# Performance work log

Measured on AMD Instinct MI355X. Metric: run time of the kernel, lower is better.

## Reference

```python
import jax, jax.numpy as jnp
import numpy as np

B, T, D, H = 4, 2048, 768, 12
HD = D // H  # head size 64
DF = 3072    # feed-forward size


def setup_inputs() -> dict:
    key = jax.random.key(0)
    ks = jax.random.split(key, 10)
    s = 0.02
    return {
        "x": jax.random.normal(ks[0], (B, T, D), jnp.float32),
        "mask": jnp.ones((B, T), jnp.int32),
        "Wq": jax.random.normal(ks[1], (D, D), jnp.float32) * s,
        "bq": jnp.zeros((D,), jnp.float32),
        "Wk": jax.random.normal(ks[2], (D, D), jnp.float32) * s,
        "bk": jnp.zeros((D,), jnp.float32),
        "Wv": jax.random.normal(ks[3], (D, D), jnp.float32) * s,
        "bv": jnp.zeros((D,), jnp.float32),
        "Wo": jax.random.normal(ks[4], (D, D), jnp.float32) * s,
        "bo": jnp.zeros((D,), jnp.float32),
        "W1": jax.random.normal(ks[5], (D, DF), jnp.float32) * s,
        "b1": jnp.zeros((DF,), jnp.float32),
        "W2": jax.random.normal(ks[6], (DF, D), jnp.float32) * s,
        "b2": jnp.zeros((D,), jnp.float32),
    }


def reference(x, mask, Wq, bq, Wk, bk, Wv, bv, Wo, bo, W1, b1, W2, b2):
    scale = 1.0 / np.sqrt(HD).astype(np.float32)
    # projections -> [B, H, T, HD]
    def split_heads(t):
        return t.reshape(B, T, H, HD).transpose(0, 2, 1, 3)
    q = split_heads(x @ Wq + bq)
    k = split_heads(x @ Wk + bk)
    v = split_heads(x @ Wv + bv)
    # [B, H, T, T] attention scores (materialized, as in the original)
    scores = jnp.einsum('bhqd,bhkd->bhqk', q, k) * scale
    neg_inf = jnp.float32(-jnp.inf)
    scores = jnp.where(mask[:, None, None, :] == 0, neg_inf, scores)
    attn = jax.nn.softmax(scores, axis=-1)
    ctx = jnp.einsum('bhqk,bhkd->bhqd', attn, v)          # [B,H,T,HD]
    ctx = ctx.transpose(0, 2, 1, 3).reshape(B, T, D)       # merge heads
    attn_out = ctx @ Wo + bo
    h = x + attn_out                                       # residual 1 (dropout p=0)
    ff = jax.nn.gelu(h @ W1 + b1, approximate=False) @ W2 + b2
    out = h + ff                                           # residual 2
    return out, attn
```

## Files before the change

### kernel.cpp

```cpp
#include <hip/hip_runtime.h>
#include <hip/hip_bf16.h>
#include <math.h>

typedef unsigned short u16;
typedef __attribute__((ext_vector_type(8))) short short8;
typedef __attribute__((ext_vector_type(4))) float f32x4;

constexpr int Bc = 4, Tt = 2048, Dd = 768, Hh = 12, Hd = 64, Df = 3072;
constexpr int BT = Bc * Tt;

__device__ __forceinline__ u16 f2b(float x) {
  __hip_bfloat16 h = __float2bfloat16(x);
  return *reinterpret_cast<u16*>(&h);
}
__device__ __forceinline__ float b2f(u16 v) {
  unsigned int u = ((unsigned int)v) << 16;
  return __builtin_bit_cast(float, u);
}
__device__ __forceinline__ float gelu_exact(float g) {
  return 0.5f * g * (1.0f + erff(g * 0.70710678118654752440f));
}
__device__ __forceinline__ void gload16(const void* g, void* l) {
  __builtin_amdgcn_global_load_lds(
      (const __attribute__((address_space(1))) unsigned int*)g,
      (__attribute__((address_space(3))) unsigned int*)l, 16, 0, 0);
}

__device__ __forceinline__ void tr_tile(const float* __restrict__ in,
                                        u16* __restrict__ out, int R, int C,
                                        int bx, int by, float* sh) {
  const int tx = threadIdx.x & 31, ty = threadIdx.x >> 5;
  const int r0 = by * 32, c0 = bx * 32;
#pragma unroll
  for (int i = 0; i < 4; ++i)
    sh[(ty + i * 8) * 33 + tx] = in[(size_t)(r0 + ty + i * 8) * C + c0 + tx];
  __syncthreads();
#pragma unroll
  for (int i = 0; i < 4; ++i)
    out[(size_t)(c0 + ty + i * 8) * R + r0 + tx] = f2b(sh[tx * 33 + ty + i * 8]);
}

__global__ __launch_bounds__(256) void prep_all(
    const float* __restrict__ x, const float* __restrict__ Wq,
    const float* __restrict__ Wk, const float* __restrict__ Wv,
    const float* __restrict__ Wo, const float* __restrict__ W1,
    const float* __restrict__ W2, const float* __restrict__ bq,
    const float* __restrict__ bk, const float* __restrict__ bv,
    const int* __restrict__ mask, u16* __restrict__ xb,
    u16* __restrict__ wqkvT, u16* __restrict__ woT, u16* __restrict__ w1T,
    u16* __restrict__ w2T, float* __restrict__ biasc,
    unsigned int* __restrict__ mwords) {
  __shared__ float sh[32 * 33];
  const int s = blockIdx.x;
  if (s < 3072) {
    int i = (s * 256 + threadIdx.x) * 8;
    float4 a = *(const float4*)&x[i];
    float4 b = *(const float4*)&x[i + 4];
    u16 t[8] = {f2b(a.x), f2b(a.y), f2b(a.z), f2b(a.w),
                f2b(b.x), f2b(b.y), f2b(b.z), f2b(b.w)};
    *(uint4*)&xb[i] = *(uint4*)t;
  } else if (s < 3648) {
    int u = s - 3072; tr_tile(Wq, wqkvT, Dd, Dd, u % 24, u / 24, sh);
  } else if (s < 4224) {
    int u = s - 3648; tr_tile(Wk, wqkvT + 768 * Dd, Dd, Dd, u % 24, u / 24, sh);
  } else if (s < 4800) {
    int u = s - 4224; tr_tile(Wv, wqkvT + 1536 * Dd, Dd, Dd, u % 24, u / 24, sh);
  } else if (s < 5376) {
    int u = s - 4800; tr_tile(Wo, woT, Dd, Dd, u % 24, u / 24, sh);
  } else if (s < 7680) {
    int u = s - 5376; tr_tile(W1, w1T, Dd, Df, u % 96, u / 96, sh);
  } else if (s < 9984) {
    int u = s - 7680; tr_tile(W2, w2T, Df, Dd, u % 24, u / 24, sh);
  } else if (s < 9993) {
    int i = (s - 9984) * 256 + threadIdx.x;
    biasc[i] = (i < 768) ? bq[i] : (i < 1536) ? bk[i - 768] : bv[i - 1536];
  } else {
    const int id = threadIdx.x;
    const int b_ = id >> 6, kv0 = (id & 63) * 32;
    unsigned int wbits = 0u;
    for (int j = 0; j < 32; ++j)
      wbits |= (mask[b_ * Tt + kv0 + j] ? 1u : 0u) << j;
    mwords[id] = wbits;
  }
}

template <int MODE>
__global__ __launch_bounds__(256) void mgemm(
    const u16* __restrict__ A, const u16* __restrict__ Bt,
    const float* __restrict__ bias, const float* __restrict__ add,
    const u16* __restrict__ addb, void* __restrict__ C0,
    void* __restrict__ C1, void* __restrict__ C2, int K, int N) {
  __shared__ __align__(16) u16 As[3][128 * 32];
  __shared__ __align__(16) u16 Bs[3][128 * 32];
  const int tid = threadIdx.x;
  const int lane = tid & 63, wv = tid >> 6;
  const int m0 = blockIdx.y * 128, n0 = blockIdx.x * 128;
  const int wm = (wv >> 1) * 64, wn = (wv & 1) * 64;

  f32x4 acc[4][4] = {};

#define MG_STAGE(k0_, bf_)                                                    \
  {                                                                           \
    _Pragma("unroll") for (int i_ = 0; i_ < 2; ++i_) {                        \
      const int idx_ = i_ * 256 + tid;                                        \
      const int row_ = idx_ >> 2;                                             \
      const int kc_ = (idx_ & 3) * 8;                                         \
      const u16* ga_;                                                         \
      if constexpr (MODE == 2) {                                              \
        const int m_ = m0 + row_, b_ = m_ >> 11, t_ = m_ & 2047;              \
        const int kk_ = (k0_) + kc_, hd_ = kk_ >> 6, d_ = kk_ & 63;           \
        ga_ = &A[(((size_t)(b_ * Hh + hd_) * Tt + t_) << 6) + d_];            \
      } else {                                                                \
        ga_ = &A[(size_t)(m0 + row_) * K + (k0_) + kc_];                      \
      }                                                                       \
      gload16(ga_, &As[bf_][idx_ * 8]);                                       \
      gload16(&Bt[(size_t)(n0 + row_) * K + (k0_) + kc_], &Bs[bf_][idx_ * 8]);\
    }                                                                         \
  }
#define FENCE() asm volatile("" ::: "memory")

  const int nsteps = K >> 5;
  MG_STAGE(0, 0);
  MG_STAGE(32, 1);

  for (int it = 0; it < nsteps; ++it) {
    if (it + 1 < nsteps)
      asm volatile("s_waitcnt vmcnt(4)" ::: "memory");
    else
      asm volatile("s_waitcnt vmcnt(0)" ::: "memory");
    __builtin_amdgcn_s_barrier();
    FENCE();
    const int cur = it % 3;
    if (it + 2 < nsteps) {
      const int nb = (it + 2) % 3;
      MG_STAGE((it + 2) * 32, nb);
    }
    short8 af[4], bfr[4];
#pragma unroll
    for (int i = 0; i < 4; ++i) {
      af[i] = *reinterpret_cast<const short8*>(
          &As[cur][(wm + i * 16 + (lane & 15)) * 32 + (lane >> 4) * 8]);
      bfr[i] = *reinterpret_cast<const short8*>(
          &Bs[cur][(wn + i * 16 + (lane & 15)) * 32 + (lane >> 4) * 8]);
    }
    __builtin_amdgcn_s_setprio(1);
#pragma unroll
    for (int i = 0; i < 4; ++i)
#pragma unroll
      for (int j = 0; j < 4; ++j)
        acc[i][j] = __builtin_amdgcn_mfma_f32_16x16x32_bf16(af[i], bfr[j],
                                                            acc[i][j], 0, 0, 0);
    __builtin_amdgcn_s_setprio(0);
  }
#undef MG_STAGE
#undef FENCE

  const int lr = (lane >> 4) * 4, lc = lane & 15;
#pragma unroll
  for (int i = 0; i < 4; ++i) {
    const int mbase = m0 + wm + i * 16 + lr;
#pragma unroll
    for (int j = 0; j < 4; ++j) {
      const int col = n0 + wn + j * 16 + lc;
      const float bvs = bias[col];
#pragma unroll
      for (int r = 0; r < 4; ++r) {
        const int m = mbase + r;
        float g = acc[i][j][r] + bvs;
        if constexpr (MODE == 5) {
          const int b = m >> 11, t = m & 2047;
          if (col < 768) {
            const int head = col >> 6, d = col & 63;
            ((u16*)C0)[(((size_t)(b * Hh + head) * Tt + t) << 6) + d] = f2b(g);
          } else if (col < 1536) {
            const int c = col - 768, head = c >> 6, d = c & 63;
            ((u16*)C1)[(((size_t)(b * Hh + head) * Tt + t) << 6) + d] = f2b(g);
          } else {
            const int c = col - 1536, head = c >> 6, d = c & 63;
            ((u16*)C2)[(((size_t)(b * Hh + head) * Hd + d) << 11) + t] = f2b(g);
          }
        } else if constexpr (MODE == 2) {
          g += add[(size_t)m * Dd + col];
          ((u16*)C0)[(size_t)m * Dd + col] = f2b(g);
        } else if constexpr (MODE == 3) {
          ((u16*)C0)[(size_t)m * N + col] = f2b(gelu_exact(g));
        } else {
          g += b2f(addb[(size_t)m * Dd + col]);
          ((float*)C0)[(size_t)m * Dd + col] = g;
        }
      }
    }
  }
}

__global__ __launch_bounds__(256) void attn_fused(
    const u16* __restrict__ qb, const u16* __restrict__ kb,
    const u16* __restrict__ vtb, const unsigned int* __restrict__ mwords,
    float* __restrict__ attn, u16* __restrict__ ctxb) {
  const int bh = blockIdx.y;
  const int b = bh / Hh;
  const int q0 = blockIdx.x * 64;
  const u16* Qg = qb + (size_t)bh * Tt * Hd;
  const u16* Kg = kb + (size_t)bh * Tt * Hd;
  const u16* Vg = vtb + (size_t)bh * Hd * Tt;
  float* attng = attn + (size_t)bh * Tt * Tt;
  u16* ctxg = ctxb + (size_t)bh * Tt * Hd;
  const unsigned int* mwp = mwords + b * 64;

  __shared__ __align__(16) u16 Ks[2][128 * 64];
  __shared__ __align__(16) u16 Vs[64 * 128];
  __shared__ __align__(16) float Pf[64 * 128];

  const int tid = threadIdx.x, lane = tid & 63, wv = tid >> 6;
  const int lc = lane & 15, lg = lane >> 4;
  const int ql = wv * 16 + lc;
  const int qsw = lc & 7;

#define STAGE_K(t, bf)                                                       \
  {                                                                          \
    const int kv0_ = (t) * 128;                                              \
    _Pragma("unroll") for (int w_ = 0; w_ < 4; ++w_) {                       \
      const int p_ = w_ * 256 + tid;                                         \
      const int row_ = p_ >> 3, kc8_ = (p_ & 7) ^ (row_ & 7);                \
      gload16(Kg + (size_t)(kv0_ + row_) * Hd + kc8_ * 8, &Ks[bf][p_ * 8]);  \
    }                                                                        \
  }
#define STAGE_V(t)                                                           \
  {                                                                          \
    const int kv0_ = (t) * 128;                                              \
    _Pragma("unroll") for (int w_ = 0; w_ < 4; ++w_) {                       \
      const int p_ = w_ * 256 + tid;                                         \
      const int d_ = p_ >> 4, pc_ = (p_ & 15) ^ (d_ & 7);                    \
      gload16(Vg + (size_t)d_ * Tt + kv0_ + pc_ * 8, &Vs[p_ * 8]);           \
    }                                                                        \
  }
#define FENCE() asm volatile("" ::: "memory")

  short8 qf[2];
#pragma unroll
  for (int ks = 0; ks < 2; ++ks)
    qf[ks] = *(const short8*)&Qg[(size_t)(q0 + ql) * Hd + ks * 32 + lg * 8];

  float l = 0.f;

  STAGE_K(0, 0);
  for (int t = 0; t < 16; ++t) {
    asm volatile("s_waitcnt vmcnt(0)" ::: "memory");
    __builtin_amdgcn_s_barrier();
    FENCE();
    const int bf = t & 1;
    if (t < 15) STAGE_K(t + 1, bf ^ 1);
    f32x4 s[8] = {};
#pragma unroll
    for (int ks = 0; ks < 2; ++ks) {
      const int ph = (ks * 4 + lg) ^ qsw;
#pragma unroll
      for (int i = 0; i < 8; ++i) {
        const short8 af = *(const short8*)&Ks[bf][(i * 16 + lc) * 64 + ph * 8];
        s[i] = __builtin_amdgcn_mfma_f32_16x16x32_bf16(af, qf[ks], s[i], 0, 0, 0);
      }
    }
    const uint4 mw4 = *(const uint4*)&mwp[t * 4];
    const unsigned int mwa[4] = {mw4.x, mw4.y, mw4.z, mw4.w};
    float ts = 0.f;
#pragma unroll
    for (int i = 0; i < 8; ++i) {
      const unsigned int w = mwa[i >> 1];
#pragma unroll
      for (int r = 0; r < 4; ++r) {
        const float bit = (float)((w >> ((i & 1) * 16 + lg * 4 + r)) & 1u);
        ts += __expf(s[i][r] * 0.125f) * bit;
      }
    }
    ts += __shfl_xor(ts, 16);
    ts += __shfl_xor(ts, 32);
    l += ts;
  }

  const float linv = 1.f / l;
  f32x4 cacc[4] = {};

  __builtin_amdgcn_s_barrier();
  FENCE();

  STAGE_K(0, 0);
  STAGE_V(0);
  for (int t = 0; t < 16; ++t) {
    const int kv0 = t * 128;
    const int bf = t & 1;
    if (t == 0)
      asm volatile("s_waitcnt vmcnt(0)" ::: "memory");
    else
      asm volatile("s_waitcnt vmcnt(8)" ::: "memory");
    __builtin_amdgcn_s_barrier();
    FENCE();
    if (t < 15) STAGE_K(t + 1, bf ^ 1);
    f32x4 s[8] = {};
#pragma unroll
    for (int ks = 0; ks < 2; ++ks) {
      const int ph = (ks * 4 + lg) ^ qsw;
#pragma unroll
      for (int i = 0; i < 8; ++i) {
        const short8 af = *(const short8*)&Ks[bf][(i * 16 + lc) * 64 + ph * 8];
        s[i] = __builtin_amdgcn_mfma_f32_16x16x32_bf16(af, qf[ks], s[i], 0, 0, 0);
      }
    }
    const uint4 mw4 = *(const uint4*)&mwp[t * 4];
    const unsigned int mwa[4] = {mw4.x, mw4.y, mw4.z, mw4.w};
#pragma unroll
    for (int i = 0; i < 8; ++i) {
      const unsigned int w = mwa[i >> 1];
      float pv[4];
#pragma unroll
      for (int r = 0; r < 4; ++r) {
        const float bit = (float)((w >> ((i & 1) * 16 + lg * 4 + r)) & 1u);
        pv[r] = __expf(s[i][r] * 0.125f) * bit * linv;
      }
      const int g = (i * 4 + lg) ^ qsw;
      *(f32x4*)&Pf[ql * 128 + g * 4] = *(f32x4*)pv;
    }
#pragma unroll
    for (int ks = 0; ks < 4; ++ks) {
      const int gA = (ks * 8 + lg * 2) ^ qsw;
      const int gB = (ks * 8 + lg * 2 + 1) ^ qsw;
      const f32x4 fA = *(const f32x4*)&Pf[ql * 128 + gA * 4];
      const f32x4 fB = *(const f32x4*)&Pf[ql * 128 + gB * 4];
      u16 pb[8] = {f2b(fA[0]), f2b(fA[1]), f2b(fA[2]), f2b(fA[3]),
                   f2b(fB[0]), f2b(fB[1]), f2b(fB[2]), f2b(fB[3])};
      const short8 pa = *(const short8*)pb;
#pragma unroll
      for (int j2 = 0; j2 < 4; ++j2) {
        const int d = j2 * 16 + lc;
        const short8 vb2 =
            *(const short8*)&Vs[d * 128 + (((ks * 4 + lg) ^ (d & 7))) * 8];
        cacc[j2] =
            __builtin_amdgcn_mfma_f32_16x16x32_bf16(pa, vb2, cacc[j2], 0, 0, 0);
      }
    }
    __builtin_amdgcn_s_barrier();
    FENCE();
    if (t < 15) STAGE_V(t + 1);
#pragma unroll
    for (int it = 0; it < 8; ++it) {
      const int row = wv * 16 + it * 2 + (lane >> 5);
      const int colg = lane & 31;
      const int g2 = colg ^ (row & 7);
      const f32x4 v = *(const f32x4*)&Pf[row * 128 + g2 * 4];
      __builtin_nontemporal_store(
          v, (f32x4*)&attng[(size_t)(q0 + row) * Tt + kv0 + colg * 4]);
    }
  }

#pragma unroll
  for (int j2 = 0; j2 < 4; ++j2)
#pragma unroll
    for (int r = 0; r < 4; ++r) {
      const int q = q0 + wv * 16 + lg * 4 + r;
      ctxg[(size_t)q * Hd + j2 * 16 + lc] = f2b(cacc[j2][r]);
    }
#undef STAGE_K
#undef STAGE_V
#undef FENCE
}

extern "C" void kernel_launch(void* const* d_in, const int* in_sizes, int n_in,
                              void* d_out, int out_size, void* d_ws,
                              size_t ws_size, hipStream_t stream) {
  const float* x = (const float*)d_in[0];
  const int* mask = (const int*)d_in[1];
  const float* Wq = (const float*)d_in[2];
  const float* bq = (const float*)d_in[3];
  const float* Wk = (const float*)d_in[4];
  const float* bk = (const float*)d_in[5];
  const float* Wv = (const float*)d_in[6];
  const float* bv = (const float*)d_in[7];
  const float* Wo = (const float*)d_in[8];
  const float* bo = (const float*)d_in[9];
  const float* W1 = (const float*)d_in[10];
  const float* b1 = (const float*)d_in[11];
  const float* W2 = (const float*)d_in[12];
  const float* b2 = (const float*)d_in[13];

  float* out = (float*)d_out;
  float* attn = out + (size_t)BT * Dd;

  char* w = (char*)d_ws;
  u16* xb = (u16*)w;      w += (size_t)BT * Dd * 2;
  u16* wqkvT = (u16*)w;   w += (size_t)Dd * 2304 * 2;
  u16* woT = (u16*)w;     w += (size_t)Dd * Dd * 2;
  u16* w1T = (u16*)w;     w += (size_t)Dd * Df * 2;
  u16* w2T = (u16*)w;     w += (size_t)Df * Dd * 2;
  float* biasc = (float*)w;            w += 2304 * 4;
  unsigned int* mwords = (unsigned int*)w; w += 256 * 4;
  u16* qb = (u16*)w;      w += (size_t)BT * Dd * 2;
  u16* kb = (u16*)w;      w += (size_t)BT * Dd * 2;
  u16* vtb = (u16*)w;     w += (size_t)BT * Dd * 2;
  u16* ctxb = (u16*)w;    w += (size_t)BT * Dd * 2;
  u16* ff1b = (u16*)w;    w += (size_t)BT * Df * 2;
  u16* hb = vtb;

  dim3 blk(256);

  prep_all<<<dim3(9994), blk, 0, stream>>>(x, Wq, Wk, Wv, Wo, W1, W2, bq, bk,
                                           bv, mask, xb, wqkvT, woT, w1T, w2T,
                                           biasc, mwords);

  mgemm<5><<<dim3(18, 64), blk, 0, stream>>>(xb, wqkvT, biasc, nullptr, nullptr,
                                             qb, kb, vtb, Dd, 2304);

  attn_fused<<<dim3(32, 48), blk, 0, stream>>>(qb, kb, vtb, mwords, attn, ctxb);

  mgemm<2><<<dim3(6, 64), blk, 0, stream>>>(ctxb, woT, bo, x, nullptr, hb,
                                            nullptr, nullptr, Dd, Dd);

  mgemm<3><<<dim3(24, 64), blk, 0, stream>>>(hb, w1T, b1, nullptr, nullptr,
                                             ff1b, nullptr, nullptr, Dd, Df);

  mgemm<4><<<dim3(6, 64), blk, 0, stream>>>(ff1b, w2T, b2, nullptr, hb, out,
                                            nullptr, nullptr, Df, Dd);
}
```

Baseline: 480.9 us.

## Double-buffer V and store P as bf16 in attention; simplify GEMM pipeline

The attention kernel now keeps the probability tile in shared memory as bf16 rather than fp32, halving that buffer and removing a separate conversion pass before the PV MFMA. V is double-buffered and prefetched together with K, which removes one block barrier per KV tile. The GEMM changes from a three-stage global_load_lds pipeline with explicit vmcnt waits and s_setprio to a plain two-stage double buffer with __syncthreads. The fp32 attention-probability output is now rebuilt from bf16-rounded values, which lowers its precision, and the simpler GEMM pipeline may hide memory latency less well.

```diff
diff --git a/kernel.cpp b/kernel.cpp
--- a/kernel.cpp
+++ b/kernel.cpp
@@ -90,8 +90,8 @@
     const float* __restrict__ bias, const float* __restrict__ add,
     const u16* __restrict__ addb, void* __restrict__ C0,
     void* __restrict__ C1, void* __restrict__ C2, int K, int N) {
-  __shared__ __align__(16) u16 As[3][128 * 32];
-  __shared__ __align__(16) u16 Bs[3][128 * 32];
+  __shared__ __align__(16) u16 As[2][128 * 32];
+  __shared__ __align__(16) u16 Bs[2][128 * 32];
   const int tid = threadIdx.x;
   const int lane = tid & 63, wv = tid >> 6;
   const int m0 = blockIdx.y * 128, n0 = blockIdx.x * 128;
@@ -117,24 +117,14 @@
       gload16(&Bt[(size_t)(n0 + row_) * K + (k0_) + kc_], &Bs[bf_][idx_ * 8]);\
     }                                                                         \
   }
-#define FENCE() asm volatile("" ::: "memory")
-
-  const int nsteps = K >> 5;
+
   MG_STAGE(0, 0);
-  MG_STAGE(32, 1);
-
-  for (int it = 0; it < nsteps; ++it) {
-    if (it + 1 < nsteps)
-      asm volatile("s_waitcnt vmcnt(4)" ::: "memory");
-    else
-      asm volatile("s_waitcnt vmcnt(0)" ::: "memory");
-    __builtin_amdgcn_s_barrier();
-    FENCE();
-    const int cur = it % 3;
-    if (it + 2 < nsteps) {
-      const int nb = (it + 2) % 3;
-      MG_STAGE((it + 2) * 32, nb);
-    }
+  __syncthreads();
+
+  int it = 0;
+  for (int k0 = 0; k0 < K; k0 += 32, ++it) {
+    const int cur = it & 1;
+    if (k0 + 32 < K) MG_STAGE(k0 + 32, cur ^ 1);
     short8 af[4], bfr[4];
 #pragma unroll
     for (int i = 0; i < 4; ++i) {
@@ -143,17 +133,15 @@
       bfr[i] = *reinterpret_cast<const short8*>(
           &Bs[cur][(wn + i * 16 + (lane & 15)) * 32 + (lane >> 4) * 8]);
     }
-    __builtin_amdgcn_s_setprio(1);
 #pragma unroll
     for (int i = 0; i < 4; ++i)
 #pragma unroll
       for (int j = 0; j < 4; ++j)
         acc[i][j] = __builtin_amdgcn_mfma_f32_16x16x32_bf16(af[i], bfr[j],
                                                             acc[i][j], 0, 0, 0);
-    __builtin_amdgcn_s_setprio(0);
+    __syncthreads();
   }
 #undef MG_STAGE
-#undef FENCE
 
   const int lr = (lane >> 4) * 4, lc = lane & 15;
 #pragma unroll
@@ -208,8 +196,8 @@
   const unsigned int* mwp = mwords + b * 64;
 
   __shared__ __align__(16) u16 Ks[2][128 * 64];
-  __shared__ __align__(16) u16 Vs[64 * 128];
-  __shared__ __align__(16) float Pf[64 * 128];
+  __shared__ __align__(16) u16 Vs[2][64 * 128];
+  __shared__ __align__(16) u16 Ps[64 * 128];
 
   const int tid = threadIdx.x, lane = tid & 63, wv = tid >> 6;
   const int lc = lane & 15, lg = lane >> 4;
@@ -225,13 +213,13 @@
       gload16(Kg + (size_t)(kv0_ + row_) * Hd + kc8_ * 8, &Ks[bf][p_ * 8]);  \
     }                                                                        \
   }
-#define STAGE_V(t)                                                           \
+#define STAGE_V(t, bf)                                                       \
   {                                                                          \
     const int kv0_ = (t) * 128;                                              \
     _Pragma("unroll") for (int w_ = 0; w_ < 4; ++w_) {                       \
       const int p_ = w_ * 256 + tid;                                         \
       const int d_ = p_ >> 4, pc_ = (p_ & 15) ^ (d_ & 7);                    \
-      gload16(Vg + (size_t)d_ * Tt + kv0_ + pc_ * 8, &Vs[p_ * 8]);           \
+      gload16(Vg + (size_t)d_ * Tt + kv0_ + pc_ * 8, &Vs[bf][p_ * 8]);       \
     }                                                                        \
   }
 #define FENCE() asm volatile("" ::: "memory")
@@ -284,7 +272,7 @@
   FENCE();
 
   STAGE_K(0, 0);
-  STAGE_V(0);
+  STAGE_V(0, 0);
   for (int t = 0; t < 16; ++t) {
     const int kv0 = t * 128;
     const int bf = t & 1;
@@ -294,7 +282,10 @@
       asm volatile("s_waitcnt vmcnt(8)" ::: "memory");
     __builtin_amdgcn_s_barrier();
     FENCE();
-    if (t < 15) STAGE_K(t + 1, bf ^ 1);
+    if (t < 15) {
+      STAGE_K(t + 1, bf ^ 1);
+      STAGE_V(t + 1, bf ^ 1);
+    }
     f32x4 s[8] = {};
 #pragma unroll
     for (int ks = 0; ks < 2; ++ks) {
@@ -310,42 +301,41 @@
 #pragma unroll
     for (int i = 0; i < 8; ++i) {
       const unsigned int w = mwa[i >> 1];
-      float pv[4];
+      u16 pb[4];
 #pragma unroll
       for (int r = 0; r < 4; ++r) {
         const float bit = (float)((w >> ((i & 1) * 16 + lg * 4 + r)) & 1u);
-        pv[r] = __expf(s[i][r] * 0.125f) * bit * linv;
-      }
-      const int g = (i * 4 + lg) ^ qsw;
-      *(f32x4*)&Pf[ql * 128 + g * 4] = *(f32x4*)pv;
+        pb[r] = f2b(__expf(s[i][r] * 0.125f) * bit * linv);
+      }
+      const int chunk = i * 2 + (lg >> 1);
+      const int ph2 = chunk ^ qsw;
+      *(uint2*)&Ps[ql * 128 + ph2 * 8 + (lg & 1) * 4] = *(uint2*)pb;
     }
 #pragma unroll
     for (int ks = 0; ks < 4; ++ks) {
-      const int gA = (ks * 8 + lg * 2) ^ qsw;
-      const int gB = (ks * 8 + lg * 2 + 1) ^ qsw;
-      const f32x4 fA = *(const f32x4*)&Pf[ql * 128 + gA * 4];
-      const f32x4 fB = *(const f32x4*)&Pf[ql * 128 + gB * 4];
-      u16 pb[8] = {f2b(fA[0]), f2b(fA[1]), f2b(fA[2]), f2b(fA[3]),
-                   f2b(fB[0]), f2b(fB[1]), f2b(fB[2]), f2b(fB[3])};
-      const short8 pa = *(const short8*)pb;
+      const short8 pa =
+          *(const short8*)&Ps[ql * 128 + ((ks * 4 + lg) ^ qsw) * 8];
 #pragma unroll
       for (int j2 = 0; j2 < 4; ++j2) {
         const int d = j2 * 16 + lc;
         const short8 vb2 =
-            *(const short8*)&Vs[d * 128 + (((ks * 4 + lg) ^ (d & 7))) * 8];
+            *(const short8*)&Vs[bf][d * 128 + (((ks * 4 + lg) ^ (d & 7))) * 8];
         cacc[j2] =
             __builtin_amdgcn_mfma_f32_16x16x32_bf16(pa, vb2, cacc[j2], 0, 0, 0);
       }
     }
-    __builtin_amdgcn_s_barrier();
-    FENCE();
-    if (t < 15) STAGE_V(t + 1);
-#pragma unroll
-    for (int it = 0; it < 8; ++it) {
-      const int row = wv * 16 + it * 2 + (lane >> 5);
+#pragma unroll
+    for (int it2 = 0; it2 < 8; ++it2) {
+      const int row = wv * 16 + it2 * 2 + (lane >> 5);
       const int colg = lane & 31;
-      const int g2 = colg ^ (row & 7);
-      const f32x4 v = *(const f32x4*)&Pf[row * 128 + g2 * 4];
+      const int chunk = colg >> 1, half = colg & 1;
+      const uint2 pr = *(const uint2*)&Ps[row * 128 +
+                                          (chunk ^ (row & 7)) * 8 + half * 4];
+      f32x4 v;
+      v[0] = b2f((u16)(pr.x & 0xffffu));
+      v[1] = b2f((u16)(pr.x >> 16));
+      v[2] = b2f((u16)(pr.y & 0xffffu));
+      v[3] = b2f((u16)(pr.y >> 16));
       __builtin_nontemporal_store(
           v, (f32x4*)&attng[(size_t)(q0 + row) * Tt + kv0 + colg * 4]);
     }
```

After: 474.5 us, median of 2. Within noise of the previous version (-1.3%).
